# Optimization experiments

Hardware: AMD Instinct MI355X
Metric: run time of the kernel (lower is better)

## Reference

```python
import jax, jax.numpy as jnp
import numpy as np

B, S, D = 2, 2048, 1024
H = 16
HD = D // H  # 64


def setup_inputs() -> dict:
    key = jax.random.key(0)
    ks = jax.random.split(key, 9)
    scale = 1.0 / np.sqrt(D)
    x = jax.random.normal(ks[0], (B, S, D), dtype=jnp.float32)
    Wq = jax.random.normal(ks[1], (D, D), dtype=jnp.float32) * scale
    bq = jnp.zeros((D,), dtype=jnp.float32)
    Wk = jax.random.normal(ks[2], (D, D), dtype=jnp.float32) * scale
    bk = jnp.zeros((D,), dtype=jnp.float32)
    Wv = jax.random.normal(ks[3], (D, D), dtype=jnp.float32) * scale
    bv = jnp.zeros((D,), dtype=jnp.float32)
    Wo = jax.random.normal(ks[4], (D, D), dtype=jnp.float32) * scale
    bo = jnp.zeros((D,), dtype=jnp.float32)
    return {"x": x, "Wq": Wq, "bq": bq, "Wk": Wk, "bk": bk,
            "Wv": Wv, "bv": bv, "Wo": Wo, "bo": bo}


def reference(x, Wq, bq, Wk, bk, Wv, bv, Wo, bo):
    b, s, d = x.shape
    # QKV projections (PhotonicCore == dim->dim linear)
    Q = x @ Wq + bq
    K = x @ Wk + bk
    V = x @ Wv + bv
    # [B, H, S, HD]
    Q = Q.reshape(b, s, H, HD).transpose(0, 2, 1, 3)
    K = K.reshape(b, s, H, HD).transpose(0, 2, 1, 3)
    V = V.reshape(b, s, H, HD).transpose(0, 2, 1, 3)
    # full [B, H, S, S] scores, exactly as the original (unfused) module
    scores = jnp.einsum("bhqd,bhkd->bhqk", Q, K) / jnp.sqrt(jnp.asarray(HD, x.dtype))
    weights = jax.nn.softmax(scores, axis=-1)
    attn = jnp.einsum("bhqk,bhkd->bhqd", weights, V)
    attn = attn.transpose(0, 2, 1, 3).reshape(b, s, d)
    return attn @ Wo + bo
```

## Files before the change

### kernel.cpp

```cpp
#include <hip/hip_runtime.h>
#include <stdint.h>

typedef unsigned short u16;
typedef unsigned int u32;
typedef unsigned long long u64;
typedef __bf16 bf16x8 __attribute__((ext_vector_type(8)));
typedef float f32x4 __attribute__((ext_vector_type(4)));
typedef unsigned short u16x8 __attribute__((ext_vector_type(8)));
typedef unsigned short u16x4 __attribute__((ext_vector_type(4)));

#define QSCALE 0.1803368801111204f

static __device__ __forceinline__ u16 f2bf(float f) {
  unsigned u = __builtin_bit_cast(unsigned, f);
  u += 0x7fffu + ((u >> 16) & 1u);
  return (u16)(u >> 16);
}

static __device__ __forceinline__ bf16x8 ldfrag(const u16* p) {
  return *reinterpret_cast<const bf16x8*>(p);
}

static __device__ __forceinline__ void gll16(const u16* g, u16* l) {
  __builtin_amdgcn_global_load_lds(
      (const __attribute__((address_space(1))) void*)g,
      (__attribute__((address_space(3))) void*)l, 16, 0, 0);
}

static __device__ __forceinline__ u32 cvt_pk_bf16(float lo, float hi) {
  u32 r;
  asm("v_cvt_pk_bf16_f32 %0, %1, %2" : "=v"(r) : "v"(lo), "v"(hi));
  return r;
}

static __device__ __forceinline__ float fexp2(float x) {
  return __builtin_amdgcn_exp2f(x);
}

static __device__ __forceinline__ float fm3(float a, float b, float c) {
  return fmaxf(fmaxf(a, b), c);
}

__global__ __launch_bounds__(256) void prep_kernel(
    const float* __restrict__ x,
    const float* __restrict__ Wq, const float* __restrict__ Wk,
    const float* __restrict__ Wv, const float* __restrict__ Wo,
    u16* __restrict__ xb, u16* __restrict__ WT) {
  __shared__ float tile[64][65];
  int bid = blockIdx.x;
  int t = threadIdx.x;
  if (bid < 2048) {
    int i = (bid * 256 + t) * 8;
    const float4* p = reinterpret_cast<const float4*>(x + i);
    float4 a = p[0], b = p[1];
    u16x8 o;
    o[0] = f2bf(a.x); o[1] = f2bf(a.y); o[2] = f2bf(a.z); o[3] = f2bf(a.w);
    o[4] = f2bf(b.x); o[5] = f2bf(b.y); o[6] = f2bf(b.z); o[7] = f2bf(b.w);
    *reinterpret_cast<u16x8*>(xb + i) = o;
    return;
  }
  int r0 = bid - 2048;
  int z = r0 >> 8, rem = r0 & 255;
  int n0 = (rem & 15) * 64, k0 = (rem >> 4) * 64;
  const float* W = (z == 0) ? Wq : (z == 1) ? Wk : (z == 2) ? Wv : Wo;
  float wscale = (z == 0) ? QSCALE : 1.0f;
  u16* out = WT + (size_t)z * 1024 * 1024;
  int rr = t >> 4;
  int cc = (t & 15) * 4;
#pragma unroll
  for (int j = 0; j < 4; ++j) {
    int r = rr + 16 * j;
    float4 v = *reinterpret_cast<const float4*>(W + (size_t)(k0 + r) * 1024 + n0 + cc);
    tile[r][cc + 0] = v.x; tile[r][cc + 1] = v.y;
    tile[r][cc + 2] = v.z; tile[r][cc + 3] = v.w;
  }
  __syncthreads();
#pragma unroll
  for (int j = 0; j < 4; ++j) {
    int nl = rr + 16 * j;
    u16x4 o;
#pragma unroll
    for (int i2 = 0; i2 < 4; ++i2) o[i2] = f2bf(tile[cc + i2][nl] * wscale);
    *reinterpret_cast<u16x4*>(out + (size_t)(n0 + nl) * 1024 + k0 + cc) = o;
  }
}

template <int MODE>
static __device__ __forceinline__ void qkv_body(
    u16* smem, const u16* __restrict__ A, const u16* __restrict__ Wt,
    const float* __restrict__ bias, float bscale, u16* __restrict__ Out) {
  int t = threadIdx.x;
  int lane = t & 63, wave = t >> 6;
  int g = lane >> 4, c = lane & 15;
  int m0 = blockIdx.y * 128, n0 = blockIdx.x * 128;
  int wm = (wave >> 1) * 32, wn = (wave & 1) * 64;

  f32x4 acc[2][4] = {};

  const u16* Ag = A + (size_t)(m0 + (t >> 2)) * 1024 + (t & 3) * 8;
  const u16* Bg = Wt + (size_t)(n0 + (t >> 2)) * 1024 + (t & 3) * 8;

  u16* dstA = smem + t * 8;
  u16* dstB = smem + 4096 + t * 8;
  const int afo = (wm + c) * 32 + g * 8;
  const int bfo = 4096 + (wn + c) * 32 + g * 8;

  gll16(Ag, dstA);
  gll16(Bg, dstB);
  gll16(Ag + 32, dstA + 8192);
  gll16(Bg + 32, dstB + 8192);
  asm volatile("s_waitcnt vmcnt(2)" ::: "memory");
  __builtin_amdgcn_s_barrier();
  asm volatile("" ::: "memory");

  int cur = 0;
  for (int st = 0; st < 32; ++st) {
    if (st <= 29) {
      int nb = cur + 2; if (nb >= 3) nb -= 3;
      gll16(Ag + (st + 2) * 32, dstA + nb * 8192);
      gll16(Bg + (st + 2) * 32, dstB + nb * 8192);
    }
    const u16* buf = smem + cur * 8192;
    bf16x8 af[2], bfr[4];
#pragma unroll
    for (int i = 0; i < 2; ++i) af[i] = ldfrag(buf + afo + 16 * i * 32);
#pragma unroll
    for (int j = 0; j < 4; ++j) bfr[j] = ldfrag(buf + bfo + 16 * j * 32);
    __builtin_amdgcn_s_setprio(1);
#pragma unroll
    for (int i = 0; i < 2; ++i)
#pragma unroll
      for (int j = 0; j < 4; ++j) {
        if (MODE == 2)
          acc[i][j] = __builtin_amdgcn_mfma_f32_16x16x32_bf16(af[i], bfr[j], acc[i][j], 0, 0, 0);
        else
          acc[i][j] = __builtin_amdgcn_mfma_f32_16x16x32_bf16(bfr[j], af[i], acc[i][j], 0, 0, 0);
      }
    __builtin_amdgcn_s_setprio(0);

    if (st <= 29)
      asm volatile("s_waitcnt vmcnt(2)" ::: "memory");
    else if (st == 30)
      asm volatile("s_waitcnt vmcnt(0)" ::: "memory");
    if (st < 31) {
      __builtin_amdgcn_s_barrier();
      asm volatile("" ::: "memory");
    }
    ++cur; if (cur == 3) cur = 0;
  }

  if (MODE == 0) {
    int nj[4], hj[4], dj[4];
    f32x4 bbj[4];
#pragma unroll
    for (int j = 0; j < 4; ++j) {
      nj[j] = n0 + wn + 16 * j + 4 * g;
      hj[j] = nj[j] >> 6; dj[j] = nj[j] & 63;
      f32x4 bb = *reinterpret_cast<const f32x4*>(&bias[nj[j]]);
#pragma unroll
      for (int r = 0; r < 4; ++r) bbj[j][r] = bb[r] * bscale;
    }
#pragma unroll
    for (int i = 0; i < 2; ++i) {
      int m = m0 + wm + 16 * i + c;
      int b2 = m >> 11, s2 = m & 2047;
#pragma unroll
      for (int j = 0; j < 4; ++j) {
        u16x4 o4;
#pragma unroll
        for (int r = 0; r < 4; ++r) o4[r] = f2bf(acc[i][j][r] + bbj[j][r]);
        *reinterpret_cast<u16x4*>(
            Out + ((size_t)(b2 * 16 + hj[j]) * 2048 + s2) * 64 + dj[j]) = o4;
      }
    }
  } else {
    float bvj[4];
#pragma unroll
    for (int j = 0; j < 4; ++j) bvj[j] = bias[n0 + wn + 16 * j + c];
    u16* tb = smem;
    int b2 = m0 >> 11, s0 = m0 & 2047;
    int rdrow = t >> 3;
    int slot = t & 7;
    int sh_base = ((wave >> 1) & 1) * 32;
    __syncthreads();
#pragma unroll
    for (int half = 0; half < 2; ++half) {
      if ((wave >> 2) == half) {
#pragma unroll
        for (int i = 0; i < 2; ++i)
#pragma unroll
          for (int j = 0; j < 4; ++j) {
            u16x4 o4;
#pragma unroll
            for (int r = 0; r < 4; ++r) o4[r] = f2bf(acc[i][j][r] + bvj[j]);
            *reinterpret_cast<u16x4*>(
                &tb[(wn + 16 * j + c) * 72 + sh_base + 16 * i + 4 * g]) = o4;
          }
      }
      __syncthreads();
#pragma unroll
      for (int k = 0; k < 2; ++k) {
        int row = rdrow + 64 * k;
        u16x8 v = *reinterpret_cast<const u16x8*>(&tb[row * 72 + slot * 8]);
        int n = n0 + row, h2 = n >> 6, d2 = n & 63;
        *reinterpret_cast<u16x8*>(
            Out + ((size_t)(b2 * 16 + h2) * 64 + d2) * 2048 + s0 + half * 64 + slot * 8) = v;
      }
      if (half == 0) __syncthreads();
    }
  }
}

__global__ __launch_bounds__(512) void qkv_gemm_kernel(
    const u16* __restrict__ xb, const u16* __restrict__ WT,
    const float* __restrict__ bq, const float* __restrict__ bk,
    const float* __restrict__ bv,
    u16* __restrict__ Q, u16* __restrict__ K, u16* __restrict__ V) {
  __shared__ u16 smem[24576];
  int z = blockIdx.z;
  if (z == 0)      qkv_body<0>(smem, xb, WT, bq, QSCALE, Q);
  else if (z == 1) qkv_body<0>(smem, xb, WT + (size_t)1024 * 1024, bk, 1.0f, K);
  else             qkv_body<2>(smem, xb, WT + (size_t)2 * 1024 * 1024, bv, 1.0f, V);
}

__global__ __launch_bounds__(512) void oproj_kernel(
    const u16* __restrict__ A, const u16* __restrict__ Wt,
    const float* __restrict__ bias, float* __restrict__ out) {
  __shared__ u16 smem[24576];
  int t = threadIdx.x;
  int lane = t & 63, wave = t >> 6;
  int g = lane >> 4, c = lane & 15;
  int m0 = blockIdx.y * 128, n0 = blockIdx.x * 128;
  int wm = (wave >> 1) * 32, wn = (wave & 1) * 64;

  f32x4 acc[2][4] = {};

  const u16* Ag = A + (size_t)(m0 + (t >> 2)) * 1024 + (t & 3) * 8;
  const u16* Bg = Wt + (size_t)(n0 + (t >> 2)) * 1024 + (t & 3) * 8;
  u16* dstA = smem + t * 8;
  u16* dstB = smem + 4096 + t * 8;
  const int afo = (wm + c) * 32 + g * 8;
  const int bfo = 4096 + (wn + c) * 32 + g * 8;

  gll16(Ag, dstA);
  gll16(Bg, dstB);
  gll16(Ag + 32, dstA + 8192);
  gll16(Bg + 32, dstB + 8192);
  asm volatile("s_waitcnt vmcnt(2)" ::: "memory");
  __builtin_amdgcn_s_barrier();
  asm volatile("" ::: "memory");

  int cur = 0;
  for (int st = 0; st < 32; ++st) {
    if (st <= 29) {
      int nb = cur + 2; if (nb >= 3) nb -= 3;
      gll16(Ag + (st + 2) * 32, dstA + nb * 8192);
      gll16(Bg + (st + 2) * 32, dstB + nb * 8192);
    }
    const u16* buf = smem + cur * 8192;
    bf16x8 af[2], bfr[4];
#pragma unroll
    for (int i = 0; i < 2; ++i) af[i] = ldfrag(buf + afo + 16 * i * 32);
#pragma unroll
    for (int j = 0; j < 4; ++j) bfr[j] = ldfrag(buf + bfo + 16 * j * 32);
    __builtin_amdgcn_s_setprio(1);
#pragma unroll
    for (int i = 0; i < 2; ++i)
#pragma unroll
      for (int j = 0; j < 4; ++j)
        acc[i][j] = __builtin_amdgcn_mfma_f32_16x16x32_bf16(bfr[j], af[i], acc[i][j], 0, 0, 0);
    __builtin_amdgcn_s_setprio(0);

    if (st <= 29)
      asm volatile("s_waitcnt vmcnt(2)" ::: "memory");
    else if (st == 30)
      asm volatile("s_waitcnt vmcnt(0)" ::: "memory");
    if (st < 31) {
      __builtin_amdgcn_s_barrier();
      asm volatile("" ::: "memory");
    }
    ++cur; if (cur == 3) cur = 0;
  }

  f32x4 bbj[4];
#pragma unroll
  for (int j = 0; j < 4; ++j)
    bbj[j] = *reinterpret_cast<const f32x4*>(&bias[n0 + wn + 16 * j + 4 * g]);
#pragma unroll
  for (int i = 0; i < 2; ++i) {
    int m = m0 + wm + 16 * i + c;
#pragma unroll
    for (int j = 0; j < 4; ++j) {
      f32x4 v = acc[i][j] + bbj[j];
      *reinterpret_cast<f32x4*>(out + (size_t)m * 1024 + n0 + wn + 16 * j + 4 * g) = v;
    }
  }
}

__global__ __launch_bounds__(512) void attn_kernel(
    const u16* __restrict__ Q, const u16* __restrict__ K,
    const u16* __restrict__ V, u16* __restrict__ attn) {
  __shared__ u16 Kf[3][4096];
  __shared__ u16 Vt[3][4096];
  __shared__ u16 Pf[8][512];

  const int t = threadIdx.x;
  const int lane = t & 63, w = t >> 6;
  const int g = lane >> 4, c = lane & 15;

  int flat = blockIdx.x + 16 * (blockIdx.y + 16 * blockIdx.z);
  int sw = (flat & 7) * 64 + (flat >> 3);
  const int b = sw >> 8, h = (sw >> 4) & 15, q0 = (sw & 15) * 128;

  const u16* Qh = Q + ((size_t)(b * 16 + h) * 2048) * 64;
  const u16* Kh = K + ((size_t)(b * 16 + h) * 2048) * 64;
  const u16* VTh = V + ((size_t)(b * 16 + h) * 64) * 2048;

  const int qw = q0 + w * 16;
  bf16x8 qf0 = ldfrag(Qh + (size_t)(qw + c) * 64 + 8 * g);
  bf16x8 qf1 = ldfrag(Qh + (size_t)(qw + c) * 64 + 32 + 8 * g);

  bf16x8 ones;
  {
    u16x8 tmp;
#pragma unroll
    for (int l = 0; l < 8; ++l) tmp[l] = 0x3F80;
    ones = __builtin_bit_cast(bf16x8, tmp);
  }

  const u16* ksrc = Kh + (size_t)(16 * ((w >> 1) & 3) + c) * 64 + 32 * (w & 1) + 8 * g;
  const u16* vsrc = VTh + (size_t)(8 * w + (lane >> 3)) * 2048 +
                    (((lane & 7) ^ ((lane >> 3) & 7)) * 8);

  const int koff = g * 128 + c * 8;
  int vb_off[2];
#pragma unroll
  for (int m = 0; m < 2; ++m)
    vb_off[m] = c * 64 + (((4 * m + g) ^ (c & 7)) * 8);
  const int pa_off = (g * 16 + c) * 8;

  f32x4 o[4] = {};
  f32x4 lsum = {};
  float mrow = -3e38f;

  gll16(ksrc, &Kf[0][t * 8]);
  gll16(vsrc, &Vt[0][t * 8]);
  gll16(ksrc + 4096, &Kf[1][t * 8]);
  gll16(vsrc + 64, &Vt[1][t * 8]);
  asm volatile("s_waitcnt vmcnt(2)" ::: "memory");
  __builtin_amdgcn_s_barrier();
  asm volatile("" ::: "memory");

  int cur = 0;
  for (int tt32 = 0; tt32 < 32; ++tt32) {
    if (tt32 <= 29) {
      int nb = cur + 2; if (nb >= 3) nb -= 3;
      gll16(ksrc + (size_t)(tt32 + 2) * 4096, &Kf[nb][t * 8]);
      gll16(vsrc + (size_t)(tt32 + 2) * 64, &Vt[nb][t * 8]);
    }

    const u16* kb = &Kf[cur][koff];
    f32x4 st[4];
    __builtin_amdgcn_s_setprio(1);
#pragma unroll
    for (int t4 = 0; t4 < 4; ++t4) {
      f32x4 acc = {};
      acc = __builtin_amdgcn_mfma_f32_16x16x32_bf16(
          ldfrag(kb + t4 * 1024), qf0, acc, 0, 0, 0);
      st[t4] = __builtin_amdgcn_mfma_f32_16x16x32_bf16(
          ldfrag(kb + t4 * 1024 + 512), qf1, acc, 0, 0, 0);
    }
    __builtin_amdgcn_s_setprio(0);

    float u1 = fm3(fm3(st[0][0], st[0][1], st[0][2]),
                   fm3(st[0][3], st[1][0], st[1][1]),
                   fm3(st[1][2], st[1][3], st[2][0]));
    float u2 = fm3(fm3(st[2][1], st[2][2], st[2][3]),
                   fm3(st[3][0], st[3][1], st[3][2]), st[3][3]);
    float tm = fmaxf(u1, u2);
    tm = fmaxf(tm, __shfl_xor(tm, 16));
    tm = fmaxf(tm, __shfl_xor(tm, 32));
    const bool grow = __any(tm > mrow + 8.0f);
    if (grow) {
      float nm = fmaxf(mrow, tm);
      float f = fexp2(mrow - nm);
      mrow = nm;
#pragma unroll
      for (int r = 0; r < 4; ++r) {
        float fr = __shfl(f, 4 * g + r);
        lsum[r] *= fr;
#pragma unroll
        for (int j = 0; j < 4; ++j) o[j][r] *= fr;
      }
    }
#pragma unroll
    for (int t4 = 0; t4 < 4; ++t4)
#pragma unroll
      for (int r = 0; r < 4; ++r) st[t4][r] = fexp2(st[t4][r] - mrow);

    u32* pd = (u32*)&Pf[w][0];
#pragma unroll
    for (int m = 0; m < 2; ++m) {
#pragma unroll
      for (int tp = 0; tp < 2; ++tp) {
        int t4 = 2 * m + tp;
        u32 w0 = cvt_pk_bf16(st[t4][0], st[t4][1]);
        u32 w1 = cvt_pk_bf16(st[t4][2], st[t4][3]);
        int gp = (2 * t4 + (g >> 1)) & 3;
        int base = (gp * 16 + c) * 4 + 2 * (g & 1);
        *reinterpret_cast<u64*>(&pd[base]) = (u64)w0 | ((u64)w1 << 32);
      }
      bf16x8 pa = ldfrag(&Pf[w][pa_off]);
      __builtin_amdgcn_s_setprio(1);
#pragma unroll
      for (int j = 0; j < 4; ++j) {
        bf16x8 vb = ldfrag(&Vt[cur][vb_off[m] + j * 1024]);
        o[j] = __builtin_amdgcn_mfma_f32_16x16x32_bf16(pa, vb, o[j], 0, 0, 0);
      }
      lsum = __builtin_amdgcn_mfma_f32_16x16x32_bf16(pa, ones, lsum, 0, 0, 0);
      __builtin_amdgcn_s_setprio(0);
    }

    if (tt32 <= 29)
      asm volatile("s_waitcnt vmcnt(2)" ::: "memory");
    else if (tt32 == 30)
      asm volatile("s_waitcnt vmcnt(0)" ::: "memory");
    if (tt32 < 31) {
      __builtin_amdgcn_s_barrier();
      asm volatile("" ::: "memory");
    }
    ++cur; if (cur == 3) cur = 0;
  }

  float rinv[4];
#pragma unroll
  for (int r = 0; r < 4; ++r) rinv[r] = 1.f / lsum[r];
#pragma unroll
  for (int j = 0; j < 4; ++j)
#pragma unroll
    for (int r = 0; r < 4; ++r) {
      int s = qw + 4 * g + r;
      attn[(size_t)(b * 2048 + s) * 1024 + h * 64 + 16 * j + c] = f2bf(o[j][r] * rinv[r]);
    }
}

extern "C" void kernel_launch(void* const* d_in, const int* in_sizes, int n_in,
                              void* d_out, int out_size, void* d_ws, size_t ws_size,
                              hipStream_t stream) {
  const float* x  = (const float*)d_in[0];
  const float* Wq = (const float*)d_in[1];
  const float* bq = (const float*)d_in[2];
  const float* Wk = (const float*)d_in[3];
  const float* bk = (const float*)d_in[4];
  const float* Wv = (const float*)d_in[5];
  const float* bv = (const float*)d_in[6];
  const float* Wo = (const float*)d_in[7];
  const float* bo = (const float*)d_in[8];
  float* out = (float*)d_out;
  u16* ws = (u16*)d_ws;

  u16* xb    = ws;
  u16* WT    = ws + (size_t)4 * 1024 * 1024;
  u16* Qb    = ws + (size_t)8 * 1024 * 1024;
  u16* Kb    = ws + (size_t)12 * 1024 * 1024;
  u16* Vb    = ws + (size_t)16 * 1024 * 1024;
  u16* attnb = xb;

  prep_kernel<<<3072, 256, 0, stream>>>(x, Wq, Wk, Wv, Wo, xb, WT);
  qkv_gemm_kernel<<<dim3(8, 32, 3), 512, 0, stream>>>(xb, WT, bq, bk, bv, Qb, Kb, Vb);
  attn_kernel<<<dim3(16, 16, 2), 512, 0, stream>>>(Qb, Kb, Vb, attnb);
  oproj_kernel<<<dim3(8, 32), 512, 0, stream>>>(attnb, WT + (size_t)3 * 1024 * 1024, bo, out);
}
```

Measured before the change: 121.6 us.

## Process 128-key tiles per iteration with double buffering instead of 64-key triple buffering

The attention loop now handles 128 keys per iteration (16 iterations instead of 32), using two 8192-element LDS buffers for K and V rather than three 4096-element ones. This halves the number of barriers and softmax max reductions, and gives more MFMA work between synchronisations. In exchange, each iteration waits for all outstanding loads (vmcnt(0)), so prefetch lookahead drops from two tiles to one, and the larger score arrays raise register pressure.

New measurement: 122.2 us. Within noise of the previous version (+0.5%).

```diff
diff --git a/kernel.cpp b/kernel.cpp
--- a/kernel.cpp
+++ b/kernel.cpp
@@ -300,8 +300,8 @@
 __global__ __launch_bounds__(512) void attn_kernel(
     const u16* __restrict__ Q, const u16* __restrict__ K,
     const u16* __restrict__ V, u16* __restrict__ attn) {
-  __shared__ u16 Kf[3][4096];
-  __shared__ u16 Vt[3][4096];
+  __shared__ u16 Kf[2][8192];
+  __shared__ u16 Vt[2][8192];
   __shared__ u16 Pf[8][512];
 
   const int t = threadIdx.x;
@@ -328,42 +328,52 @@
     ones = __builtin_bit_cast(bf16x8, tmp);
   }
 
-  const u16* ksrc = Kh + (size_t)(16 * ((w >> 1) & 3) + c) * 64 + 32 * (w & 1) + 8 * g;
-  const u16* vsrc = VTh + (size_t)(8 * w + (lane >> 3)) * 2048 +
-                    (((lane & 7) ^ ((lane >> 3) & 7)) * 8);
+  const u16* ksrc0;
+  {
+    int u = t;
+    int cc = u & 15, gg = (u >> 4) & 3, uu = (u >> 6) & 1, t4 = u >> 7;
+    ksrc0 = Kh + (size_t)(16 * t4 + cc) * 64 + 32 * uu + 8 * gg;
+  }
+  const u16* vsrc0 = VTh + (size_t)(t >> 4) * 2048 + (((t & 15) ^ ((t >> 4) & 7)) * 8);
+  u16* kdst = (u16*)&Kf[0][0] + t * 8;
+  u16* vdst = (u16*)&Vt[0][0] + t * 8;
 
   const int koff = g * 128 + c * 8;
-  int vb_off[2];
-#pragma unroll
-  for (int m = 0; m < 2; ++m)
-    vb_off[m] = c * 64 + (((4 * m + g) ^ (c & 7)) * 8);
+  int vb_off[4];
+#pragma unroll
+  for (int mh = 0; mh < 4; ++mh)
+    vb_off[mh] = c * 128 + (((4 * mh + g) ^ (c & 7)) * 8);
   const int pa_off = (g * 16 + c) * 8;
 
   f32x4 o[4] = {};
   f32x4 lsum = {};
   float mrow = -3e38f;
 
-  gll16(ksrc, &Kf[0][t * 8]);
-  gll16(vsrc, &Vt[0][t * 8]);
-  gll16(ksrc + 4096, &Kf[1][t * 8]);
-  gll16(vsrc + 64, &Vt[1][t * 8]);
-  asm volatile("s_waitcnt vmcnt(2)" ::: "memory");
+  gll16(ksrc0, kdst);
+  gll16(ksrc0 + 4096, kdst + 4096);
+  gll16(vsrc0, vdst);
+  gll16(vsrc0 + 65536, vdst + 4096);
+  asm volatile("s_waitcnt vmcnt(0)" ::: "memory");
   __builtin_amdgcn_s_barrier();
   asm volatile("" ::: "memory");
 
   int cur = 0;
-  for (int tt32 = 0; tt32 < 32; ++tt32) {
-    if (tt32 <= 29) {
-      int nb = cur + 2; if (nb >= 3) nb -= 3;
-      gll16(ksrc + (size_t)(tt32 + 2) * 4096, &Kf[nb][t * 8]);
-      gll16(vsrc + (size_t)(tt32 + 2) * 64, &Vt[nb][t * 8]);
+  for (int tt = 0; tt < 16; ++tt) {
+    if (tt <= 14) {
+      size_t kadv = (size_t)(tt + 1) * 8192;
+      size_t vadv = (size_t)(tt + 1) * 128;
+      int nb = cur ^ 1;
+      gll16(ksrc0 + kadv, kdst + nb * 8192);
+      gll16(ksrc0 + kadv + 4096, kdst + nb * 8192 + 4096);
+      gll16(vsrc0 + vadv, vdst + nb * 8192);
+      gll16(vsrc0 + vadv + 65536, vdst + nb * 8192 + 4096);
     }
 
     const u16* kb = &Kf[cur][koff];
-    f32x4 st[4];
+    f32x4 st[8];
     __builtin_amdgcn_s_setprio(1);
 #pragma unroll
-    for (int t4 = 0; t4 < 4; ++t4) {
+    for (int t4 = 0; t4 < 8; ++t4) {
       f32x4 acc = {};
       acc = __builtin_amdgcn_mfma_f32_16x16x32_bf16(
           ldfrag(kb + t4 * 1024), qf0, acc, 0, 0, 0);
@@ -372,12 +382,12 @@
     }
     __builtin_amdgcn_s_setprio(0);
 
-    float u1 = fm3(fm3(st[0][0], st[0][1], st[0][2]),
-                   fm3(st[0][3], st[1][0], st[1][1]),
-                   fm3(st[1][2], st[1][3], st[2][0]));
-    float u2 = fm3(fm3(st[2][1], st[2][2], st[2][3]),
-                   fm3(st[3][0], st[3][1], st[3][2]), st[3][3]);
-    float tm = fmaxf(u1, u2);
+    float tmq[8];
+#pragma unroll
+    for (int t4 = 0; t4 < 8; ++t4)
+      tmq[t4] = fmaxf(fm3(st[t4][0], st[t4][1], st[t4][2]), st[t4][3]);
+    float tm = fmaxf(fm3(fm3(tmq[0], tmq[1], tmq[2]), fm3(tmq[3], tmq[4], tmq[5]), tmq[6]),
+                     tmq[7]);
     tm = fmaxf(tm, __shfl_xor(tm, 16));
     tm = fmaxf(tm, __shfl_xor(tm, 32));
     const bool grow = __any(tm > mrow + 8.0f);
@@ -394,19 +404,19 @@
       }
     }
 #pragma unroll
-    for (int t4 = 0; t4 < 4; ++t4)
+    for (int t4 = 0; t4 < 8; ++t4)
 #pragma unroll
       for (int r = 0; r < 4; ++r) st[t4][r] = fexp2(st[t4][r] - mrow);
 
     u32* pd = (u32*)&Pf[w][0];
 #pragma unroll
-    for (int m = 0; m < 2; ++m) {
+    for (int mh = 0; mh < 4; ++mh) {
 #pragma unroll
       for (int tp = 0; tp < 2; ++tp) {
-        int t4 = 2 * m + tp;
+        int t4 = 2 * mh + tp;
         u32 w0 = cvt_pk_bf16(st[t4][0], st[t4][1]);
         u32 w1 = cvt_pk_bf16(st[t4][2], st[t4][3]);
-        int gp = (2 * t4 + (g >> 1)) & 3;
+        int gp = 2 * (t4 & 1) + (g >> 1);
         int base = (gp * 16 + c) * 4 + 2 * (g & 1);
         *reinterpret_cast<u64*>(&pd[base]) = (u64)w0 | ((u64)w1 << 32);
       }
@@ -414,22 +424,20 @@
       __builtin_amdgcn_s_setprio(1);
 #pragma unroll
       for (int j = 0; j < 4; ++j) {
-        bf16x8 vb = ldfrag(&Vt[cur][vb_off[m] + j * 1024]);
+        bf16x8 vb = ldfrag(&Vt[cur][vb_off[mh] + j * 2048]);
         o[j] = __builtin_amdgcn_mfma_f32_16x16x32_bf16(pa, vb, o[j], 0, 0, 0);
       }
       lsum = __builtin_amdgcn_mfma_f32_16x16x32_bf16(pa, ones, lsum, 0, 0, 0);
       __builtin_amdgcn_s_setprio(0);
     }
 
-    if (tt32 <= 29)
-      asm volatile("s_waitcnt vmcnt(2)" ::: "memory");
-    else if (tt32 == 30)
+    if (tt <= 14)
       asm volatile("s_waitcnt vmcnt(0)" ::: "memory");
-    if (tt32 < 31) {
+    if (tt < 15) {
       __builtin_amdgcn_s_barrier();
       asm volatile("" ::: "memory");
     }
-    ++cur; if (cur == 3) cur = 0;
+    cur ^= 1;
   }
 
   float rinv[4];
```

## Load K fragments directly into registers and double-buffer V in LDS

Applied to the files above, without the earlier changes.

The attention kernel stops staging K tiles through shared memory. Each wave now loads its K fragments straight from global memory into registers one tile ahead, while V keeps an LDS pipeline that drops from three buffers to two. The aim is to cut LDS traffic and footprint so more blocks fit per CU (launch bounds now request 4). The cost is that all 8 waves read the same K from global/L2 redundantly, more registers are held live, and a full vmcnt(0) wait each iteration leaves less load latency hidden.

Result: slower. 188.7 us (+55.3%).

```diff
diff --git a/kernel.cpp b/kernel.cpp
--- a/kernel.cpp
+++ b/kernel.cpp
@@ -297,11 +297,10 @@
   }
 }
 
-__global__ __launch_bounds__(512) void attn_kernel(
+__global__ __launch_bounds__(512, 4) void attn_kernel(
     const u16* __restrict__ Q, const u16* __restrict__ K,
     const u16* __restrict__ V, u16* __restrict__ attn) {
-  __shared__ u16 Kf[3][4096];
-  __shared__ u16 Vt[3][4096];
+  __shared__ u16 Vt[2][4096];
   __shared__ u16 Pf[8][512];
 
   const int t = threadIdx.x;
@@ -328,11 +327,12 @@
     ones = __builtin_bit_cast(bf16x8, tmp);
   }
 
-  const u16* ksrc = Kh + (size_t)(16 * ((w >> 1) & 3) + c) * 64 + 32 * (w & 1) + 8 * g;
+  const u16* kbase = Kh + (size_t)c * 64 + 8 * g;
+
   const u16* vsrc = VTh + (size_t)(8 * w + (lane >> 3)) * 2048 +
                     (((lane & 7) ^ ((lane >> 3) & 7)) * 8);
-
-  const int koff = g * 128 + c * 8;
+  u16* vdst = (u16*)&Vt[0][0] + t * 8;
+
   int vb_off[2];
 #pragma unroll
   for (int m = 0; m < 2; ++m)
@@ -343,34 +343,39 @@
   f32x4 lsum = {};
   float mrow = -3e38f;
 
-  gll16(ksrc, &Kf[0][t * 8]);
-  gll16(vsrc, &Vt[0][t * 8]);
-  gll16(ksrc + 4096, &Kf[1][t * 8]);
-  gll16(vsrc + 64, &Vt[1][t * 8]);
-  asm volatile("s_waitcnt vmcnt(2)" ::: "memory");
+  gll16(vsrc, vdst);
+  asm volatile("s_waitcnt vmcnt(0)" ::: "memory");
   __builtin_amdgcn_s_barrier();
   asm volatile("" ::: "memory");
 
+  bf16x8 kr[4][2];
+#pragma unroll
+  for (int t4 = 0; t4 < 4; ++t4)
+#pragma unroll
+    for (int u = 0; u < 2; ++u)
+      kr[t4][u] = ldfrag(kbase + t4 * 1024 + u * 32);
+
   int cur = 0;
-  for (int tt32 = 0; tt32 < 32; ++tt32) {
-    if (tt32 <= 29) {
-      int nb = cur + 2; if (nb >= 3) nb -= 3;
-      gll16(ksrc + (size_t)(tt32 + 2) * 4096, &Kf[nb][t * 8]);
-      gll16(vsrc + (size_t)(tt32 + 2) * 64, &Vt[nb][t * 8]);
-    }
-
-    const u16* kb = &Kf[cur][koff];
+  for (int tt = 0; tt < 32; ++tt) {
     f32x4 st[4];
     __builtin_amdgcn_s_setprio(1);
 #pragma unroll
     for (int t4 = 0; t4 < 4; ++t4) {
       f32x4 acc = {};
-      acc = __builtin_amdgcn_mfma_f32_16x16x32_bf16(
-          ldfrag(kb + t4 * 1024), qf0, acc, 0, 0, 0);
-      st[t4] = __builtin_amdgcn_mfma_f32_16x16x32_bf16(
-          ldfrag(kb + t4 * 1024 + 512), qf1, acc, 0, 0, 0);
+      acc = __builtin_amdgcn_mfma_f32_16x16x32_bf16(kr[t4][0], qf0, acc, 0, 0, 0);
+      st[t4] = __builtin_amdgcn_mfma_f32_16x16x32_bf16(kr[t4][1], qf1, acc, 0, 0, 0);
     }
     __builtin_amdgcn_s_setprio(0);
+
+    if (tt < 31) {
+      gll16(vsrc + (size_t)(tt + 1) * 64, vdst + (cur ^ 1) * 4096);
+      const u16* kb2 = kbase + (size_t)(tt + 1) * 4096;
+#pragma unroll
+      for (int t4 = 0; t4 < 4; ++t4)
+#pragma unroll
+        for (int u = 0; u < 2; ++u)
+          kr[t4][u] = ldfrag(kb2 + t4 * 1024 + u * 32);
+    }
 
     float u1 = fm3(fm3(st[0][0], st[0][1], st[0][2]),
                    fm3(st[0][3], st[1][0], st[1][1]),
@@ -421,15 +426,12 @@
       __builtin_amdgcn_s_setprio(0);
     }
 
-    if (tt32 <= 29)
-      asm volatile("s_waitcnt vmcnt(2)" ::: "memory");
-    else if (tt32 == 30)
+    if (tt < 31) {
       asm volatile("s_waitcnt vmcnt(0)" ::: "memory");
-    if (tt32 < 31) {
       __builtin_amdgcn_s_barrier();
       asm volatile("" ::: "memory");
     }
-    ++cur; if (cur == 3) cur = 0;
+    cur ^= 1;
   }
 
   float rinv[4];
```
